# Performance work log

Measured on AMD Instinct MI355X. Metric: run time of the kernel, lower is better.

The kernel has to match this reference:

```python
import jax, jax.numpy as jnp
import numpy as np
from jax import lax

B, S, PH, N = 4, 512, 4096, 16384
D, G, H, L, FF, GS = 1024, 128, 8, 4, 4096, 32
HD = D // H


def setup_inputs() -> dict:
    key = jax.random.key(0)
    ks = list(jax.random.split(key, 16))
    r = lambda k, sh: jax.random.normal(k, sh, jnp.float32) * 0.02
    return {
        'last_hidden': jax.random.normal(ks[0], (B, S, PH), jnp.float32),
        'current_pointcloud': jax.random.normal(ks[1], (B, N, 3), jnp.float32),
        'fp_w': r(ks[2], (D, PH)), 'fp_b': jnp.zeros((D,), jnp.float32),
        'sp_w': r(ks[3], (G * D, D)), 'sp_b': jnp.zeros((G * D,), jnp.float32),
        'pos_embed': r(ks[4], (1, G, D)),
        'ln1_w': jnp.ones((L, D), jnp.float32), 'ln1_b': jnp.zeros((L, D), jnp.float32),
        'in_w': r(ks[5], (L, 3 * D, D)), 'in_b': jnp.zeros((L, 3 * D), jnp.float32),
        'out_w': r(ks[6], (L, D, D)), 'out_b': jnp.zeros((L, D), jnp.float32),
        'ln2_w': jnp.ones((L, D), jnp.float32), 'ln2_b': jnp.zeros((L, D), jnp.float32),
        'mlp_w1': r(ks[7], (L, FF, D)), 'mlp_b1': jnp.zeros((L, FF), jnp.float32),
        'mlp_w2': r(ks[8], (L, D, FF)), 'mlp_b2': jnp.zeros((L, D), jnp.float32),
        'c1_w': r(ks[9], (D, D)), 'c1_b': jnp.zeros((D,), jnp.float32),
        'bn_g': jnp.ones((D,), jnp.float32), 'bn_beta': jnp.zeros((D,), jnp.float32),
        'bn_m': jnp.zeros((D,), jnp.float32), 'bn_v': jnp.ones((D,), jnp.float32),
        'c2_w': r(ks[10], (3 * GS, D)), 'c2_b': jnp.zeros((3 * GS,), jnp.float32),
    }


def _ln(x, w, b):
    m = jnp.mean(x, -1, keepdims=True)
    v = jnp.mean(jnp.square(x - m), -1, keepdims=True)
    return (x - m) * lax.rsqrt(v + 1e-5) * w + b


def _fps(xyz, num_samples):
    # iterative farthest point sampling; deterministic start index 0
    Bb, Nn, _ = xyz.shape
    dist0 = jnp.full((Bb, Nn), 1e10, xyz.dtype)
    far0 = jnp.zeros((Bb,), jnp.int32)

    def step(carry, _):
        dist, far = carry
        centroid = jnp.take_along_axis(xyz, far[:, None, None], axis=1)  # [B,1,3]
        d = jnp.sum(jnp.square(xyz - centroid), -1)                      # [B,N]
        dist = jnp.minimum(dist, d)
        return (dist, jnp.argmax(dist, -1).astype(jnp.int32)), far

    _, cents = lax.scan(step, (dist0, far0), None, length=num_samples)
    cents = cents.T  # [B, num_samples]
    return jnp.take_along_axis(xyz, cents[:, :, None], axis=1)  # [B,num_samples,3]


def reference(last_hidden, current_pointcloud, fp_w, fp_b, sp_w, sp_b, pos_embed,
              ln1_w, ln1_b, in_w, in_b, out_w, out_b, ln2_w, ln2_b,
              mlp_w1, mlp_b1, mlp_w2, mlp_b2,
              c1_w, c1_b, bn_g, bn_beta, bn_m, bn_v, c2_w, c2_b):
    bsz = last_hidden.shape[0]
    agg = jnp.mean(last_hidden @ fp_w.T + fp_b, axis=1)          # [B,D]
    x = (agg @ sp_w.T + sp_b).reshape(bsz, G, D)                 # [B,G,D]
    centers = _fps(current_pointcloud, G)                        # [B,G,3]
    scale = 1.0 / np.sqrt(HD).astype(np.float32)

    def block(x, p):
        l1w, l1b, iw, ib, ow, ob, l2w, l2b, w1, b1, w2, b2 = p
        xn = _ln(x + pos_embed, l1w, l1b)
        qkv = xn @ iw.T + ib                                     # [B,G,3D]
        q, k, v = jnp.split(qkv, 3, axis=-1)
        hsp = lambda t: t.reshape(bsz, G, H, HD).transpose(0, 2, 1, 3)
        q, k, v = hsp(q), hsp(k), hsp(v)
        a = jax.nn.softmax(jnp.einsum('bhqd,bhkd->bhqk', q, k) * scale, axis=-1)
        o = jnp.einsum('bhqk,bhkd->bhqd', a, v).transpose(0, 2, 1, 3).reshape(bsz, G, D)
        x = x + o @ ow.T + ob
        h = jax.nn.gelu(_ln(x, l2w, l2b) @ w1.T + b1, approximate=False)
        return x + h @ w2.T + b2, None

    x, _ = lax.scan(block, x, (ln1_w, ln1_b, in_w, in_b, out_w, out_b,
                               ln2_w, ln2_b, mlp_w1, mlp_b1, mlp_w2, mlp_b2))

    # future_predictor: 1x1 conv == per-token linear; BN in eval mode
    h = x @ c1_w.T + c1_b
    h = jax.nn.relu((h - bn_m) * lax.rsqrt(bn_v + 1e-5) * bn_g + bn_beta)
    deltas = (h @ c2_w.T + c2_b).reshape(bsz * G, GS, 3)
    pred = deltas + centers.reshape(bsz * G, 1, 3)
    return pred.reshape(bsz, G * GS, 3)
```

## Files before the change

### kernel.cpp

```cpp
#include <hip/hip_runtime.h>
#include <hip/hip_bf16.h>
#include <math.h>


typedef __bf16 bf16x8_t __attribute__((ext_vector_type(8)));
typedef float  f32x4_t  __attribute__((ext_vector_type(4)));

__device__ __forceinline__ float wredsum(float v){
#pragma unroll
  for (int o = 32; o; o >>= 1) v += __shfl_down(v, o, 64);
  return v;
}

__device__ __forceinline__ bf16x8_t pack8(float4 a, float4 b){
  bf16x8_t v;
  v[0]=(__bf16)a.x; v[1]=(__bf16)a.y; v[2]=(__bf16)a.z; v[3]=(__bf16)a.w;
  v[4]=(__bf16)b.x; v[5]=(__bf16)b.y; v[6]=(__bf16)b.z; v[7]=(__bf16)b.w;
  return v;
}

__device__ __forceinline__ void gload16(const void* g, void* l){
  __builtin_amdgcn_global_load_lds((const __attribute__((address_space(1))) unsigned int*)g,
                                   (__attribute__((address_space(3))) unsigned int*)l, 16, 0, 0);
}

__global__ __launch_bounds__(1024) void fused_front(
  const float* __restrict__ pc, float* __restrict__ centers,
  const float* __restrict__ agg, const float* __restrict__ spw,
  const float* __restrict__ spb, float* __restrict__ x,
  const float* __restrict__ inw, const float* __restrict__ outw,
  const float* __restrict__ w1, const float* __restrict__ w2,
  const float* __restrict__ c1w, __bf16* __restrict__ wbf)
{
  const int bid = blockIdx.x;
  const int tid = threadIdx.x;
  if (bid < 4){
    const int b = bid;
    const int lane = tid & 63;
    const float* base = pc + (size_t)b * 16384 * 3;
    float px[16], py[16], pz[16], dist[16];
    {
      union { float4 v4[12]; float f[48]; } u;
      const float4* src = (const float4*)(base + tid * 48);
#pragma unroll
      for (int q = 0; q < 12; ++q) u.v4[q] = src[q];
#pragma unroll
      for (int j = 0; j < 16; ++j){
        px[j] = u.f[j*3]; py[j] = u.f[j*3+1]; pz[j] = u.f[j*3+2];
        dist[j] = 1e10f;
      }
    }
    __shared__ unsigned long long keyslot[128];
    for (int i = tid; i < 128; i += 1024) keyslot[i] = 0ULL;
    __syncthreads();
    float cx = base[0], cy = base[1], cz = base[2];
    for (int t = 0; t < 128; ++t){
      if (tid == 0){
        centers[(b*128+t)*3+0] = cx;
        centers[(b*128+t)*3+1] = cy;
        centers[(b*128+t)*3+2] = cz;
      }
      if (t == 127) break;
      float bmax = -1.0f; int bidx = 0;
#pragma unroll
      for (int j = 0; j < 16; ++j){
        float dx = __fsub_rn(px[j], cx);
        float dy = __fsub_rn(py[j], cy);
        float dz = __fsub_rn(pz[j], cz);
        float d  = __fadd_rn(__fadd_rn(__fmul_rn(dx,dx), __fmul_rn(dy,dy)), __fmul_rn(dz,dz));
        float nd = fminf(dist[j], d);
        dist[j] = nd;
        if (nd > bmax){ bmax = nd; bidx = tid*16 + j; }
      }
      unsigned long long key = ((unsigned long long)__float_as_uint(bmax) << 32)
                             | (unsigned long long)(0xFFFFFFFFu - (unsigned)bidx);
#pragma unroll
      for (int o = 32; o; o >>= 1){
        unsigned long long ok = __shfl_down(key, o, 64);
        if (ok > key) key = ok;
      }
      if (lane == 0) atomicMax(&keyslot[t], key);
      __syncthreads();
      const unsigned long long gk = keyslot[t];
      const unsigned gidx = 0xFFFFFFFFu - (unsigned)(gk & 0xFFFFFFFFu);
      const float* cp = base + (size_t)gidx*3;
      cx = cp[0]; cy = cp[1]; cz = cp[2];
    }
  } else if (bid < 1028){
    __shared__ float ag[4096];
    for (int i = tid; i < 4096; i += 1024) ag[i] = agg[i];
    __syncthreads();
    const int wv = tid >> 6, lane = tid & 63;
    const int rbase = ((bid - 4)*16 + wv)*8;
    for (int rr = 0; rr < 8; ++rr){
      const int row = rbase + rr;
      const float* wp = spw + (size_t)row*1024 + lane*4;
      const float4 w0 = *(const float4*)(wp      );
      const float4 wq1 = *(const float4*)(wp + 256);
      const float4 wq2 = *(const float4*)(wp + 512);
      const float4 wq3 = *(const float4*)(wp + 768);
      float acc[4];
#pragma unroll
      for (int bb = 0; bb < 4; ++bb){
        const float* gp = &ag[bb*1024 + lane*4];
        const float4 g0 = *(const float4*)(gp      );
        const float4 g1 = *(const float4*)(gp + 256);
        const float4 g2 = *(const float4*)(gp + 512);
        const float4 g3 = *(const float4*)(gp + 768);
        acc[bb] = w0.x*g0.x + w0.y*g0.y + w0.z*g0.z + w0.w*g0.w
                + wq1.x*g1.x + wq1.y*g1.y + wq1.z*g1.z + wq1.w*g1.w
                + wq2.x*g2.x + wq2.y*g2.y + wq2.z*g2.z + wq2.w*g2.w
                + wq3.x*g3.x + wq3.y*g3.y + wq3.z*g3.z + wq3.w*g3.w;
      }
      float a0 = wredsum(acc[0]);
      float a1 = wredsum(acc[1]);
      float a2 = wredsum(acc[2]);
      float a3 = wredsum(acc[3]);
      if (lane == 0){
        const float bias = spb[row];
        x[(size_t)0*131072 + row] = a0 + bias;
        x[(size_t)1*131072 + row] = a1 + bias;
        x[(size_t)2*131072 + row] = a2 + bias;
        x[(size_t)3*131072 + row] = a3 + bias;
      }
    }
  } else {
    const size_t t = (size_t)(bid - 1028)*1024 + tid;
    const size_t i = t*8;
    const float* src;
    if (i < 50331648){
      const size_t l = i / 12582912, r = i - l*12582912;
      if (r < 3145728)       src = inw  + l*3145728 + r;
      else if (r < 4194304)  src = outw + l*1048576 + (r-3145728);
      else if (r < 8388608)  src = w1   + l*4194304 + (r-4194304);
      else                   src = w2   + l*4194304 + (r-8388608);
    } else src = c1w + (i - 50331648);
    float4 a = *(const float4*)src, bq = *(const float4*)(src+4);
    *(bf16x8_t*)(wbf + i) = pack8(a, bq);
  }
}

__global__ __launch_bounds__(256) void partial_kernel(const float* __restrict__ lh,
                                                      float* __restrict__ part){
  const int ph = blockIdx.x*256 + threadIdx.x;
  const int sc = blockIdx.y, b = blockIdx.z;
  const float* p = lh + ((size_t)b*512 + sc*64)*4096 + ph;
  float s0=0,s1=0,s2=0,s3=0;
  for (int j = 0; j < 64; j += 4){
    s0 += p[(size_t)(j+0)*4096];
    s1 += p[(size_t)(j+1)*4096];
    s2 += p[(size_t)(j+2)*4096];
    s3 += p[(size_t)(j+3)*4096];
  }
  part[(size_t)(b*8+sc)*4096 + ph] = (s0+s1)+(s2+s3);
}

__global__ __launch_bounds__(256) void combine_kernel(const float* __restrict__ part,
                                                      float* __restrict__ mlh){
  const int i = blockIdx.x*256 + threadIdx.x;
  const int b = i >> 12, ph = i & 4095;
  float s = 0;
#pragma unroll
  for (int sc = 0; sc < 8; ++sc) s += part[(size_t)(b*8+sc)*4096 + ph];
  mlh[i] = s * (1.0f/512.0f);
}

__global__ __launch_bounds__(256) void agg_kernel(const float* __restrict__ mlh,
                                                  const float* __restrict__ fpw,
                                                  const float* __restrict__ fpb,
                                                  float* __restrict__ agg){
  const int o = blockIdx.x*4 + (threadIdx.x>>6);
  const int lane = threadIdx.x & 63;
  const int b = o >> 10, d = o & 1023;
  const float* mp = mlh + b*4096;
  const float* wp = fpw + (size_t)d*4096;
  float s = 0;
#pragma unroll 4
  for (int j = 0; j < 64; ++j){
    int ph = lane + j*64;
    s += mp[ph] * wp[ph];
  }
  s = wredsum(s);
  if (lane == 0) agg[o] = s + fpb[d];
}

__global__ __launch_bounds__(256) void ln_kernel(const float* __restrict__ x,
                                                 const float* __restrict__ pos,
                                                 const float* __restrict__ w,
                                                 const float* __restrict__ bb,
                                                 __bf16* __restrict__ out){
  const int tok = blockIdx.x, g = tok & 127, t = threadIdx.x;
  const int lane = t & 63, wv = t >> 6;
  const float* xr = x + (size_t)tok*1024;
  float v[4];
#pragma unroll
  for (int j = 0; j < 4; ++j){
    int d = t + j*256;
    float val = xr[d];
    if (pos) val += pos[g*1024 + d];
    v[j] = val;
  }
  __shared__ float r1[4], r2[4];
  float s = wredsum(v[0]+v[1]+v[2]+v[3]);
  if (lane == 0) r1[wv] = s;
  __syncthreads();
  const float mean = (r1[0]+r1[1]+r1[2]+r1[3]) * (1.0f/1024.0f);
  float sq = 0;
#pragma unroll
  for (int j = 0; j < 4; ++j){ float d0 = v[j]-mean; sq += d0*d0; }
  sq = wredsum(sq);
  if (lane == 0) r2[wv] = sq;
  __syncthreads();
  const float var = (r2[0]+r2[1]+r2[2]+r2[3]) * (1.0f/1024.0f);
  const float rs = rsqrtf(var + 1e-5f);
#pragma unroll
  for (int j = 0; j < 4; ++j){
    int d = t + j*256;
    out[(size_t)tok*1024 + d] = (__bf16)((v[j]-mean)*rs*w[d] + bb[d]);
  }
}

__global__ __launch_bounds__(256) void gemm_sk(
  const __bf16* __restrict__ A, const __bf16* __restrict__ W,
  float* __restrict__ parts, int M, int N, int K, int kc)
{
  __shared__ __bf16 As[128*64];
  __shared__ __bf16 Ws[128*64];
  const int n0 = blockIdx.x*128, m0 = blockIdx.y*128, z = blockIdx.z;
  const int tid = threadIdx.x;
  const int lane = tid & 63, w = tid >> 6;
  const int wm = w >> 1, wn = w & 1;
  const int lr = lane & 15, g = lane >> 4;
  const int kbeg = z*kc, kend = kbeg + kc;
  const int c0 = tid, c1 = tid+256, c2 = tid+512, c3 = tid+768;
  const int r0 = c0>>3, r1 = c1>>3, r2 = c2>>3, r3 = c3>>3;
  const int s0 = ((c0&7) ^ (r0&7))*8, s1 = ((c1&7) ^ (r1&7))*8;
  const int s2 = ((c2&7) ^ (r2&7))*8, s3 = ((c3&7) ^ (r3&7))*8;
  const __bf16* pa0 = A + (size_t)(m0+r0)*K + kbeg + s0;
  const __bf16* pa1 = A + (size_t)(m0+r1)*K + kbeg + s1;
  const __bf16* pa2 = A + (size_t)(m0+r2)*K + kbeg + s2;
  const __bf16* pa3 = A + (size_t)(m0+r3)*K + kbeg + s3;
  const __bf16* pw0 = W + (size_t)(n0+r0)*K + kbeg + s0;
  const __bf16* pw1 = W + (size_t)(n0+r1)*K + kbeg + s1;
  const __bf16* pw2 = W + (size_t)(n0+r2)*K + kbeg + s2;
  const __bf16* pw3 = W + (size_t)(n0+r3)*K + kbeg + s3;
  f32x4_t acc[4][4] = {};
  for (int k0 = 0; k0 < kc; k0 += 64){
    __syncthreads();
    gload16(pa0 + k0, &As[c0*8]);
    gload16(pa1 + k0, &As[c1*8]);
    gload16(pa2 + k0, &As[c2*8]);
    gload16(pa3 + k0, &As[c3*8]);
    gload16(pw0 + k0, &Ws[c0*8]);
    gload16(pw1 + k0, &Ws[c1*8]);
    gload16(pw2 + k0, &Ws[c2*8]);
    gload16(pw3 + k0, &Ws[c3*8]);
    __syncthreads();
#pragma unroll
    for (int ks2 = 0; ks2 < 2; ++ks2){
      bf16x8_t af[4], bf[4];
#pragma unroll
      for (int f = 0; f < 4; ++f){
        const int ra = wm*64 + f*16 + lr;
        const int rb = wn*64 + f*16 + lr;
        const int lq = ks2*4 + g;
        af[f] = *(bf16x8_t*)&As[ra*64 + (lq ^ (ra&7))*8];
        bf[f] = *(bf16x8_t*)&Ws[rb*64 + (lq ^ (rb&7))*8];
      }
#pragma unroll
      for (int i = 0; i < 4; ++i)
#pragma unroll
        for (int j = 0; j < 4; ++j)
          acc[i][j] = __builtin_amdgcn_mfma_f32_16x16x32_bf16(af[i], bf[j], acc[i][j], 0, 0, 0);
    }
  }
  float* C = parts + (size_t)z*M*N;
#pragma unroll
  for (int i = 0; i < 4; ++i)
#pragma unroll
    for (int j = 0; j < 4; ++j)
#pragma unroll
      for (int r = 0; r < 4; ++r){
        const int row = m0 + wm*64 + i*16 + g*4 + r;
        const int col = n0 + wn*64 + j*16 + lr;
        C[(size_t)row*N + col] = acc[i][j][r];
      }
}

__global__ __launch_bounds__(256) void comb_qkv(const float* __restrict__ parts,
                                                const float* __restrict__ bias,
                                                __bf16* __restrict__ out){
  const int i = blockIdx.x*256 + threadIdx.x;
  const int col = i % 3072;
  out[i] = (__bf16)(parts[i] + parts[1572864 + i] + bias[col]);
}

__global__ __launch_bounds__(256) void comb_gelu(const float* __restrict__ parts,
                                                 const float* __restrict__ bias,
                                                 __bf16* __restrict__ out){
  const int i = blockIdx.x*256 + threadIdx.x;
  const int col = i & 4095;
  float v = parts[i] + parts[2097152 + i] + bias[col];
  v = v * 0.5f * (1.0f + erff(v * 0.70710678118654752440f));
  out[i] = (__bf16)v;
}

template<int MODE>
__global__ __launch_bounds__(256) void comb_res_ln(const float* __restrict__ parts, int nsplit,
                                                   const float* __restrict__ bias,
                                                   const float* __restrict__ pos,
                                                   const float* __restrict__ lw,
                                                   const float* __restrict__ lb,
                                                   float* __restrict__ x,
                                                   __bf16* __restrict__ xn){
  const int tok = blockIdx.x, gi = tok & 127, t = threadIdx.x;
  const int lane = t & 63, wv = t >> 6;
  float v[4];
#pragma unroll
  for (int j = 0; j < 4; ++j){
    const int d = t + j*256;
    const size_t idx = (size_t)tok*1024 + d;
    float s = 0;
    for (int z = 0; z < nsplit; ++z) s += parts[(size_t)z*524288 + idx];
    float val = x[idx] + s + bias[d];
    x[idx] = val;
    v[j] = val;
  }
  if (MODE == 2){
#pragma unroll
    for (int j = 0; j < 4; ++j){
      const int d = t + j*256;
      xn[(size_t)tok*1024 + d] = (__bf16)v[j];
    }
    return;
  }
  float u[4];
#pragma unroll
  for (int j = 0; j < 4; ++j){
    const int d = t + j*256;
    u[j] = v[j] + (MODE == 1 ? pos[gi*1024 + d] : 0.0f);
  }
  __shared__ float r1[4], r2[4];
  float s1 = wredsum(u[0]+u[1]+u[2]+u[3]);
  if (lane == 0) r1[wv] = s1;
  __syncthreads();
  const float mean = (r1[0]+r1[1]+r1[2]+r1[3]) * (1.0f/1024.0f);
  float sq = 0;
#pragma unroll
  for (int j = 0; j < 4; ++j){ float d0 = u[j]-mean; sq += d0*d0; }
  sq = wredsum(sq);
  if (lane == 0) r2[wv] = sq;
  __syncthreads();
  const float var = (r2[0]+r2[1]+r2[2]+r2[3]) * (1.0f/1024.0f);
  const float rs = rsqrtf(var + 1e-5f);
#pragma unroll
  for (int j = 0; j < 4; ++j){
    const int d = t + j*256;
    xn[(size_t)tok*1024 + d] = (__bf16)((u[j]-mean)*rs*lw[d] + lb[d]);
  }
}

__global__ __launch_bounds__(256) void attn_fused(const __bf16* __restrict__ qkv,
                                                  __bf16* __restrict__ O){
  const int bh = blockIdx.x >> 1, half = blockIdx.x & 1;
  const int b = bh>>3, h = bh&7;
  const int tid = threadIdx.x, w = tid>>6, lane = tid&63;
  const int lr = lane&15, g = lane>>4;
  __shared__ __bf16 vt[128*128];
  __shared__ __bf16 pl[4*2048];
  {
    const int n = tid >> 1, kh = tid & 1;
    const __bf16* vbase = qkv + (size_t)(b*128)*3072 + 2048 + h*128 + n;
#pragma unroll
    for (int jb = 0; jb < 8; ++jb){
      bf16x8_t pk;
#pragma unroll
      for (int e = 0; e < 8; ++e) pk[e] = vbase[(size_t)(kh*64 + jb*8 + e)*3072];
      const int cb = kh*8 + jb;
      *(bf16x8_t*)&vt[n*128 + ((cb ^ (n&7)) * 8)] = pk;
    }
  }
  const __bf16* qbase = qkv + (size_t)(b*128)*3072 + h*128;
  const __bf16* kbase = qbase + 1024;
  const int qrow0 = half*64 + w*16;
  f32x4_t acc[8] = {};
#pragma unroll
  for (int ks = 0; ks < 4; ++ks){
    bf16x8_t aq, bk[8];
    aq = *(const bf16x8_t*)(qbase + (size_t)(qrow0 + lr)*3072 + ks*32 + g*8);
#pragma unroll
    for (int j = 0; j < 8; ++j)
      bk[j] = *(const bf16x8_t*)(kbase + (size_t)(j*16 + lr)*3072 + ks*32 + g*8);
#pragma unroll
    for (int j = 0; j < 8; ++j)
      acc[j] = __builtin_amdgcn_mfma_f32_16x16x32_bf16(aq, bk[j], acc[j], 0, 0, 0);
  }
  __syncthreads();
  const float scale = 0.088388347648318447f;
#pragma unroll
  for (int r = 0; r < 4; ++r){
    const int row = g*4 + r;
    float sv[8];
    float mx = -1e30f;
#pragma unroll
    for (int j = 0; j < 8; ++j){ sv[j] = acc[j][r]*scale; mx = fmaxf(mx, sv[j]); }
#pragma unroll
    for (int o = 1; o < 16; o <<= 1) mx = fmaxf(mx, __shfl_xor(mx, o, 64));
    float s = 0;
#pragma unroll
    for (int j = 0; j < 8; ++j){ sv[j] = expf(sv[j]-mx); s += sv[j]; }
#pragma unroll
    for (int o = 1; o < 16; o <<= 1) s += __shfl_xor(s, o, 64);
    const float inv = 1.0f/s;
#pragma unroll
    for (int j = 0; j < 8; ++j){
      const int col = j*16 + lr;
      const int slot = (col>>3) ^ (row&7);
      pl[w*2048 + row*128 + slot*8 + (lr&7)] = (__bf16)(sv[j]*inv);
    }
  }
  __syncthreads();
  f32x4_t acc2[8] = {};
#pragma unroll
  for (int ks = 0; ks < 4; ++ks){
    bf16x8_t ap, bv[8];
    {
      const int row = lr;
      const int slot = (ks*4 + g) ^ (row&7);
      ap = *(bf16x8_t*)&pl[w*2048 + row*128 + slot*8];
    }
#pragma unroll
    for (int j = 0; j < 8; ++j){
      const int rowv = j*16 + lr;
      const int cb = ks*4 + g;
      bv[j] = *(bf16x8_t*)&vt[rowv*128 + ((cb ^ (rowv&7))*8)];
    }
#pragma unroll
    for (int j = 0; j < 8; ++j)
      acc2[j] = __builtin_amdgcn_mfma_f32_16x16x32_bf16(ap, bv[j], acc2[j], 0, 0, 0);
  }
#pragma unroll
  for (int j = 0; j < 8; ++j)
#pragma unroll
    for (int r = 0; r < 4; ++r){
      const int row = qrow0 + g*4 + r;
      const int col = j*16 + lr;
      O[(size_t)(b*128+row)*1024 + h*128 + col] = (__bf16)acc2[j][r];
    }
}

__global__ __launch_bounds__(256) void head_kernel(const float* __restrict__ parts,
                                                   const float* __restrict__ c1b,
                                                   const float* __restrict__ bnm,
                                                   const float* __restrict__ bnv,
                                                   const float* __restrict__ bng,
                                                   const float* __restrict__ bnb,
                                                   const float* __restrict__ c2w,
                                                   const float* __restrict__ c2b,
                                                   const float* __restrict__ centers,
                                                   float* __restrict__ out){
  const int tok = blockIdx.x, t = threadIdx.x;
  const int wv = t >> 6, lane = t & 63;
  __shared__ float hrow[1024];
#pragma unroll
  for (int j = 0; j < 4; ++j){
    const int d = t + j*256;
    const size_t idx = (size_t)tok*1024 + d;
    float s = 0;
#pragma unroll
    for (int z = 0; z < 8; ++z) s += parts[(size_t)z*524288 + idx];
    float v = s + c1b[d];
    v = (v - bnm[d]) * rsqrtf(bnv[d] + 1e-5f) * bng[d] + bnb[d];
    hrow[d] = fmaxf(v, 0.0f);
  }
  __syncthreads();
  for (int i = 0; i < 24; ++i){
    const int n = wv*24 + i;
    const float* wp = c2w + (size_t)n*1024;
    float s = 0;
#pragma unroll 4
    for (int j = 0; j < 16; ++j){
      const int k = lane + j*64;
      s += hrow[k] * wp[k];
    }
    s = wredsum(s);
    if (lane == 0) out[(size_t)tok*96 + n] = s + c2b[n] + centers[tok*3 + (n % 3)];
  }
}

extern "C" void kernel_launch(void* const* d_in, const int* in_sizes, int n_in,
                              void* d_out, int out_size, void* d_ws, size_t ws_size,
                              hipStream_t stream){
  const float* lh   = (const float*)d_in[0];
  const float* pc   = (const float*)d_in[1];
  const float* fpw  = (const float*)d_in[2];
  const float* fpb  = (const float*)d_in[3];
  const float* spw  = (const float*)d_in[4];
  const float* spb  = (const float*)d_in[5];
  const float* pos  = (const float*)d_in[6];
  const float* ln1w = (const float*)d_in[7];
  const float* ln1b = (const float*)d_in[8];
  const float* inw  = (const float*)d_in[9];
  const float* inb  = (const float*)d_in[10];
  const float* outw = (const float*)d_in[11];
  const float* outb = (const float*)d_in[12];
  const float* ln2w = (const float*)d_in[13];
  const float* ln2b = (const float*)d_in[14];
  const float* w1   = (const float*)d_in[15];
  const float* b1   = (const float*)d_in[16];
  const float* w2   = (const float*)d_in[17];
  const float* b2   = (const float*)d_in[18];
  const float* c1w  = (const float*)d_in[19];
  const float* c1b  = (const float*)d_in[20];
  const float* bng  = (const float*)d_in[21];
  const float* bnbt = (const float*)d_in[22];
  const float* bnm  = (const float*)d_in[23];
  const float* bnv  = (const float*)d_in[24];
  const float* c2w  = (const float*)d_in[25];
  const float* c2b  = (const float*)d_in[26];
  float* out = (float*)d_out;

  float* f = (float*)d_ws;
  float* parts = f;              f += 16*524288;
  float* part  = f;              f += 131072;
  float* mlh   = f;              f += 16384;
  float* agg   = f;              f += 4096;
  float* x     = f;              f += 524288;
  float* cent  = f;              f += 2048;
  __bf16* bfp = (__bf16*)f;
  __bf16* xn   = bfp;            bfp += 524288;
  __bf16* qkv  = bfp;            bfp += 1572864;
  __bf16* obuf = bfp;            bfp += 524288;
  __bf16* hbf  = bfp;            bfp += 2097152;
  __bf16* xbf  = bfp;            bfp += 524288;
  __bf16* wbf  = bfp;            bfp += 51380224;

  partial_kernel<<<dim3(16,8,4), 256, 0, stream>>>(lh, part);
  combine_kernel<<<64, 256, 0, stream>>>(part, mlh);
  agg_kernel<<<1024, 256, 0, stream>>>(mlh, fpw, fpb, agg);
  fused_front<<<7300, 1024, 0, stream>>>(pc, cent, agg, spw, spb, x,
                                         inw, outw, w1, w2, c1w, wbf);
  ln_kernel<<<512, 256, 0, stream>>>(x, pos, ln1w, ln1b, xn);

  for (int l = 0; l < 4; ++l){
    const __bf16* wl = wbf + (size_t)l*12582912;
    gemm_sk<<<dim3(24,4,2), 256, 0, stream>>>(xn, wl, parts, 512, 3072, 1024, 512);
    comb_qkv<<<6144, 256, 0, stream>>>(parts, inb + l*3072, qkv);
    attn_fused<<<64, 256, 0, stream>>>(qkv, obuf);
    gemm_sk<<<dim3(8,4,8), 256, 0, stream>>>(obuf, wl + 3145728, parts, 512, 1024, 1024, 128);
    comb_res_ln<0><<<512, 256, 0, stream>>>(parts, 8, outb + l*1024, nullptr,
                                            ln2w + l*1024, ln2b + l*1024, x, xn);
    gemm_sk<<<dim3(32,4,2), 256, 0, stream>>>(xn, wl + 4194304, parts, 512, 4096, 1024, 512);
    comb_gelu<<<8192, 256, 0, stream>>>(parts, b1 + l*4096, hbf);
    gemm_sk<<<dim3(8,4,8), 256, 0, stream>>>(hbf, wl + 8388608, parts, 512, 1024, 4096, 512);
    if (l < 3)
      comb_res_ln<1><<<512, 256, 0, stream>>>(parts, 8, b2 + l*1024, pos,
                                              ln1w + (l+1)*1024, ln1b + (l+1)*1024, x, xn);
    else
      comb_res_ln<2><<<512, 256, 0, stream>>>(parts, 8, b2 + l*1024, nullptr,
                                              nullptr, nullptr, x, xbf);
  }

  gemm_sk<<<dim3(8,4,8), 256, 0, stream>>>(xbf, wbf + 50331648, parts, 512, 1024, 1024, 128);
  head_kernel<<<512, 256, 0, stream>>>(parts, c1b, bnm, bnv, bng, bnbt, c2w, c2b, cent, out);
}
```

Measured before the change: 798.7 us.

## Defer per-layer weight bf16 conversion into the attention kernel launches

The fp32-to-bf16 conversion of every layer's weights, previously done all at once in the front kernel, is now split up. The front kernel converts only layer 0, and each layer's attention launch carries extra blocks that convert the next layer's weights (or the head conv weights on the last layer). This spreads conversion traffic across the layer loop and uses idle CUs during the small 64-block attention kernel. The cost is that the attention kernel now runs much longer, because 6144 extra conversion blocks share its launch.

```diff
diff --git a/kernel.cpp b/kernel.cpp
--- a/kernel.cpp
+++ b/kernel.cpp
@@ -30,7 +30,7 @@
   const float* __restrict__ spb, float* __restrict__ x,
   const float* __restrict__ inw, const float* __restrict__ outw,
   const float* __restrict__ w1, const float* __restrict__ w2,
-  const float* __restrict__ c1w, __bf16* __restrict__ wbf)
+  __bf16* __restrict__ wbf)
 {
   const int bid = blockIdx.x;
   const int tid = threadIdx.x;
@@ -128,13 +128,10 @@
     const size_t t = (size_t)(bid - 1028)*1024 + tid;
     const size_t i = t*8;
     const float* src;
-    if (i < 50331648){
-      const size_t l = i / 12582912, r = i - l*12582912;
-      if (r < 3145728)       src = inw  + l*3145728 + r;
-      else if (r < 4194304)  src = outw + l*1048576 + (r-3145728);
-      else if (r < 8388608)  src = w1   + l*4194304 + (r-4194304);
-      else                   src = w2   + l*4194304 + (r-8388608);
-    } else src = c1w + (i - 50331648);
+    if (i < 3145728)       src = inw  + i;
+    else if (i < 4194304)  src = outw + (i-3145728);
+    else if (i < 8388608)  src = w1   + (i-4194304);
+    else                   src = w2   + (i-8388608);
     float4 a = *(const float4*)src, bq = *(const float4*)(src+4);
     *(bf16x8_t*)(wbf + i) = pack8(a, bq);
   }
@@ -231,7 +228,7 @@
   const int lane = tid & 63, w = tid >> 6;
   const int wm = w >> 1, wn = w & 1;
   const int lr = lane & 15, g = lane >> 4;
-  const int kbeg = z*kc, kend = kbeg + kc;
+  const int kbeg = z*kc;
   const int c0 = tid, c1 = tid+256, c2 = tid+512, c3 = tid+768;
   const int r0 = c0>>3, r1 = c1>>3, r2 = c2>>3, r3 = c3>>3;
   const int s0 = ((c0&7) ^ (r0&7))*8, s1 = ((c1&7) ^ (r1&7))*8;
@@ -361,7 +358,31 @@
 }
 
 __global__ __launch_bounds__(256) void attn_fused(const __bf16* __restrict__ qkv,
-                                                  __bf16* __restrict__ O){
+                                                  __bf16* __restrict__ O,
+                                                  const float* __restrict__ cs0,
+                                                  const float* __restrict__ cs1,
+                                                  const float* __restrict__ cs2,
+                                                  const float* __restrict__ cs3,
+                                                  __bf16* __restrict__ cdst,
+                                                  int nch){
+  if (blockIdx.x >= 64){
+    const int t = (blockIdx.x - 64)*256 + threadIdx.x;
+    if (t < nch){
+      const size_t i = (size_t)t*8;
+      const float* src;
+      if (cs1 == nullptr){
+        src = cs0 + i;
+      } else {
+        if (i < 3145728)       src = cs0 + i;
+        else if (i < 4194304)  src = cs1 + (i-3145728);
+        else if (i < 8388608)  src = cs2 + (i-4194304);
+        else                   src = cs3 + (i-8388608);
+      }
+      float4 a = *(const float4*)src, bq = *(const float4*)(src+4);
+      *(bf16x8_t*)(cdst + i) = pack8(a, bq);
+    }
+    return;
+  }
   const int bh = blockIdx.x >> 1, half = blockIdx.x & 1;
   const int b = bh>>3, h = bh&7;
   const int tid = threadIdx.x, w = tid>>6, lane = tid&63;
@@ -538,15 +559,22 @@
   partial_kernel<<<dim3(16,8,4), 256, 0, stream>>>(lh, part);
   combine_kernel<<<64, 256, 0, stream>>>(part, mlh);
   agg_kernel<<<1024, 256, 0, stream>>>(mlh, fpw, fpb, agg);
-  fused_front<<<7300, 1024, 0, stream>>>(pc, cent, agg, spw, spb, x,
-                                         inw, outw, w1, w2, c1w, wbf);
+  fused_front<<<2564, 1024, 0, stream>>>(pc, cent, agg, spw, spb, x,
+                                         inw, outw, w1, w2, wbf);
   ln_kernel<<<512, 256, 0, stream>>>(x, pos, ln1w, ln1b, xn);
 
   for (int l = 0; l < 4; ++l){
     const __bf16* wl = wbf + (size_t)l*12582912;
     gemm_sk<<<dim3(24,4,2), 256, 0, stream>>>(xn, wl, parts, 512, 3072, 1024, 512);
     comb_qkv<<<6144, 256, 0, stream>>>(parts, inb + l*3072, qkv);
-    attn_fused<<<64, 256, 0, stream>>>(qkv, obuf);
+    if (l < 3)
+      attn_fused<<<64 + 6144, 256, 0, stream>>>(qkv, obuf,
+          inw + (size_t)(l+1)*3145728, outw + (size_t)(l+1)*1048576,
+          w1 + (size_t)(l+1)*4194304, w2 + (size_t)(l+1)*4194304,
+          wbf + (size_t)(l+1)*12582912, 1572864);
+    else
+      attn_fused<<<64 + 512, 256, 0, stream>>>(qkv, obuf,
+          c1w, nullptr, nullptr, nullptr, wbf + 50331648, 131072);
     gemm_sk<<<dim3(8,4,8), 256, 0, stream>>>(obuf, wl + 3145728, parts, 512, 1024, 1024, 128);
     comb_res_ln<0><<<512, 256, 0, stream>>>(parts, 8, outb + l*1024, nullptr,
                                             ln2w + l*1024, ln2b + l*1024, x, xn);
```

Measured after the change: 794.1 us. Within noise of the previous version (-0.6%).
